# Performance work log

Hardware: AMD Instinct MI355X
Metric: run time of the kernel (lower is better)

## Reference

```python
import jax, jax.numpy as jnp
from jax import lax
import numpy as np

L = 2          # num_delimiter_layers
H = 8          # num q/kv heads
MIN_CL = 3
MAX_CL = 16

def rms_norm(x, w, eps=1e-6):
    return x * lax.rsqrt(jnp.mean(x * x, axis=-1, keepdims=True) + eps) * w

def rope(t):
    # t: [B, H, S, Dh], GPT-NeoX style half-split rotation, theta=10000
    Dh, S = t.shape[-1], t.shape[-2]
    half = Dh // 2
    inv = 1.0 / (10000.0 ** (jnp.arange(half, dtype=jnp.float32) / half))
    fr = jnp.arange(S, dtype=jnp.float32)[:, None] * inv  # [S, half]
    cos, sin = jnp.cos(fr), jnp.sin(fr)
    t1, t2 = t[..., :half], t[..., half:]
    return jnp.concatenate([t1 * cos - t2 * sin, t1 * sin + t2 * cos], axis=-1)

def chunk_ids_one(flags):
    # flags: [S] bool (probs > 0.5). Returns per-position chunk id and num chunks.
    S = flags.shape[0]
    # ends take value p+1 for flagged p; fallback to a single end at S-1 if none.
    has_end = jnp.zeros(S + 1, bool).at[1:].set(flags)
    fallback = jnp.zeros(S + 1, bool).at[S - 1].set(True)
    has_end = jnp.where(flags.any(), has_end, fallback)
    idx = jnp.where(has_end, jnp.arange(S + 1), S + 1)  # S+1 = sentinel > any cap
    nxt = lax.associative_scan(jnp.minimum, idx, reverse=True)  # nxt[e] = min end >= e
    def step(carry, t):
        cur_end, cid = carry
        def new(_):
            cap = jnp.minimum(t + MAX_CL, S)
            e = nxt[t + 1]                       # smallest end > t
            e = jnp.where(e <= cap, e, cap)
            e = jnp.where(e - t < MIN_CL, jnp.minimum(t + MIN_CL, S), e)
            return e, cid + 1
        new_end, new_cid = lax.cond(t == cur_end, new, lambda _: (cur_end, cid), None)
        return (new_end, new_cid), new_cid
    (_, last), ids = lax.scan(step, (jnp.int32(0), jnp.int32(-1)), jnp.arange(S, dtype=jnp.int32))
    return ids, last + 1

def _forward(x, ln1, Wq, Wk, Wv, Wo, ln2, W1, W2, head_w, head_b):
    B, S, D = x.shape
    Dh = D // H
    causal = jnp.tril(jnp.ones((S, S), bool))
    scale = 1.0 / np.sqrt(Dh)
    for l in range(L):
        h = rms_norm(x, ln1[l])
        def split_heads(t):
            return t.reshape(B, S, H, Dh).transpose(0, 2, 1, 3)
        q = rope(split_heads(h @ Wq[l]))
        k = rope(split_heads(h @ Wk[l]))
        v = split_heads(h @ Wv[l])
        scores = jnp.einsum('bhqd,bhkd->bhqk', q, k) * scale
        scores = jnp.where(causal, scores, jnp.finfo(scores.dtype).min)
        attn = jax.nn.softmax(scores, axis=-1)
        o = jnp.einsum('bhqk,bhkd->bhqd', attn, v)
        o = o.transpose(0, 2, 1, 3).reshape(B, S, D)
        x = x + o @ Wo[l]
        h = rms_norm(x, ln2[l])
        x = x + jax.nn.gelu(h @ W1[l], approximate=False) @ W2[l]
    logits = (x @ head_w).squeeze(-1) + head_b[0]
    probs = jax.nn.sigmoid(logits)
    chunk_len_loss = jnp.mean(jnp.sum(probs, axis=1))
    return x, probs, chunk_len_loss

def setup_inputs():
    key = jax.random.key(0)
    ks = jax.random.split(key, 10)
    B, S, D = 4, 2048, 512
    F = 4 * D
    sc = 0.02
    return {
        'x': jax.random.normal(ks[0], (B, S, D), jnp.float32),
        'x_ids': jax.random.randint(ks[1], (B, S), 0, 256),
        'ln1': jnp.ones((L, D), jnp.float32),
        'Wq': jax.random.normal(ks[2], (L, D, D), jnp.float32) * sc,
        'Wk': jax.random.normal(ks[3], (L, D, D), jnp.float32) * sc,
        'Wv': jax.random.normal(ks[4], (L, D, D), jnp.float32) * sc,
        'Wo': jax.random.normal(ks[5], (L, D, D), jnp.float32) * sc,
        'ln2': jnp.ones((L, D), jnp.float32),
        'W1': jax.random.normal(ks[6], (L, D, F), jnp.float32) * sc,
        'W2': jax.random.normal(ks[7], (L, F, D), jnp.float32) * sc,
        'head_w': jax.random.normal(ks[8], (D, 1), jnp.float32) * sc,
        'head_b': jnp.zeros((1,), jnp.float32),
    }

def reference(x, x_ids, ln1, Wq, Wk, Wv, Wo, ln2, W1, W2, head_w, head_b):
    B, S, D = x.shape
    x_t, probs, chunk_len_loss = _forward(x, ln1, Wq, Wk, Wv, Wo, ln2, W1, W2, head_w, head_b)
    flags = probs > 0.5
    ids, n_chunks = jax.vmap(chunk_ids_one)(flags)  # ids: [B,S] int32
    # chunks partition [0,S), so block-diagonal mask == chunk-id equality
    attention_masks = ids[:, :, None] == ids[:, None, :]
    # per-batch mean chunk length = S / num_chunks (lengths sum to S)
    avg_chunk_len = jnp.mean(jnp.float32(S) / n_chunks.astype(jnp.float32))
    return (x_t, x_ids, avg_chunk_len, attention_masks, chunk_len_loss)
```

## Files before the change

kernel.cpp:

```cpp
#include <hip/hip_runtime.h>
#include <math.h>

#define S_LEN 2048
#define DMODEL 512
#define NHEAD 8
#define DH 64
#define FDIM 2048

typedef unsigned short ushort_t;
typedef __attribute__((ext_vector_type(8))) short short8_t;
typedef __attribute__((ext_vector_type(4))) float float4_t;

#define MFMA16(a, b, c) __builtin_amdgcn_mfma_f32_16x16x32_bf16(a, b, c, 0, 0, 0)



__device__ __forceinline__ ushort_t f2bf(float x) {
    unsigned u = __float_as_uint(x);
    return (ushort_t)((u + 0x7fffu + ((u >> 16) & 1u)) >> 16);
}
__device__ __forceinline__ float bf2f(ushort_t h) {
    return __uint_as_float((unsigned)h << 16);
}
__device__ __forceinline__ float gelu_f(float x) {
    return 0.5f * x * (1.0f + erff(x * 0.70710678118654752440f));
}
__device__ __forceinline__ void gl_lds16(const void* g, void* l) {
    __builtin_amdgcn_global_load_lds(
        (const __attribute__((address_space(1))) void*)g,
        (__attribute__((address_space(3))) void*)l, 16, 0, 0);
}

__device__ __forceinline__ void stage_tile(const ushort_t* __restrict__ g, int rs,
                                           ushort_t* __restrict__ s, int w, int lane) {
    #pragma unroll
    for (int j = 0; j < 2; ++j) {
        const int c = (w * 2 + j) * 64 + lane;
        const int kk = c >> 8, row = (c >> 2) & 63, q = c & 3;
        const int qs = q ^ ((row >> 1) & 3);
        gl_lds16(g + (size_t)row * rs + kk * 32 + qs * 8, s + c * 8);
    }
}

__global__ void copy_init_k(const float* __restrict__ x, const int* __restrict__ x_ids,
                            float* __restrict__ out) {
    size_t i = (size_t)blockIdx.x * blockDim.x + threadIdx.x;
    float4* o4 = (float4*)out;
    o4[i] = ((const float4*)x)[i];
    if (i < 2048) {
        int4 id4 = ((const int4*)x_ids)[i];
        o4[1048576 + i] = make_float4((float)id4.x, (float)id4.y, (float)id4.z, (float)id4.w);
    }
    if (i == 0) { out[4202496] = 0.0f; out[20979713] = 0.0f; }
}

__global__ __launch_bounds__(256) void rope_tab_k(float2* __restrict__ tab) {
    const int i = blockIdx.x * 256 + threadIdx.x;
    const int s = i >> 5, f = i & 31;
    float inv = powf(10000.0f, -(float)f * (1.0f / 32.0f));
    float sn, cs;
    sincosf((float)s * inv, &sn, &cs);
    tab[i] = make_float2(cs, sn);
}

__global__ __launch_bounds__(256) void tsplit_all_k(const float* __restrict__ Wq,
                                                    const float* __restrict__ Wk,
                                                    const float* __restrict__ Wv,
                                                    const float* __restrict__ Wo,
                                                    const float* __restrict__ W1,
                                                    const float* __restrict__ W2,
                                                    ushort_t* __restrict__ wbuf) {
    __shared__ float T[32][33];
    const int bid = blockIdx.x;
    const int l = bid / 3072;
    const int r = bid % 3072;
    ushort_t* lb = wbuf + (size_t)l * 6291456;
    const float* W; ushort_t* Thi; ushort_t* Tlo; int K, N, ntn, rr;
    if (r < 768) {
        const int which = r >> 8; rr = r & 255;
        W = (which == 0 ? Wq : which == 1 ? Wk : Wv) + (size_t)l * 262144;
        Thi = lb + which * 262144; Tlo = lb + 786432 + which * 262144;
        K = 512; N = 512; ntn = 16;
    } else if (r < 1024) {
        rr = r - 768; W = Wo + (size_t)l * 262144;
        Thi = lb + 1572864; Tlo = lb + 1835008; K = 512; N = 512; ntn = 16;
    } else if (r < 2048) {
        rr = r - 1024; W = W1 + (size_t)l * 1048576;
        Thi = lb + 2097152; Tlo = lb + 3145728; K = 512; N = 2048; ntn = 64;
    } else {
        rr = r - 2048; W = W2 + (size_t)l * 1048576;
        Thi = lb + 4194304; Tlo = lb + 5242880; K = 2048; N = 512; ntn = 16;
    }
    const int n0 = (rr % ntn) * 32, k0 = (rr / ntn) * 32;
    const int tx = threadIdx.x & 31, ty = threadIdx.x >> 5;
    #pragma unroll
    for (int i = 0; i < 4; ++i)
        T[ty + 8 * i][tx] = W[(size_t)(k0 + ty + 8 * i) * N + n0 + tx];
    __syncthreads();
    #pragma unroll
    for (int i = 0; i < 4; ++i) {
        const int n = ty + 8 * i;
        float x = T[tx][n];
        ushort_t hi = f2bf(x);
        Thi[(size_t)(n0 + n) * K + k0 + tx] = hi;
        Tlo[(size_t)(n0 + n) * K + k0 + tx] = f2bf(x - bf2f(hi));
    }
}

__global__ __launch_bounds__(256) void rmsnorm_split_k(const float* __restrict__ x,
                                                       const float* __restrict__ w,
                                                       ushort_t* __restrict__ hhi,
                                                       ushort_t* __restrict__ hlo) {
    __shared__ float red[4];
    const int tid = threadIdx.x;
    const size_t row = blockIdx.x;
    const float* xr = x + row * DMODEL;
    float2 v = *(const float2*)(xr + tid * 2);
    float ss = v.x * v.x + v.y * v.y;
    #pragma unroll
    for (int off = 32; off; off >>= 1) ss += __shfl_down(ss, off);
    if ((tid & 63) == 0) red[tid >> 6] = ss;
    __syncthreads();
    float tot = red[0] + red[1] + red[2] + red[3];
    float rs = 1.0f / sqrtf(tot * (1.0f / 512.0f) + 1e-6f);
    float2 wv = *(const float2*)(w + tid * 2);
    float y0 = v.x * rs * wv.x, y1 = v.y * rs * wv.y;
    ushort_t h0 = f2bf(y0), h1 = f2bf(y1);
    ushort_t l0 = f2bf(y0 - bf2f(h0)), l1 = f2bf(y1 - bf2f(h1));
    *(unsigned*)(hhi + row * DMODEL + tid * 2) = ((unsigned)h1 << 16) | h0;
    *(unsigned*)(hlo + row * DMODEL + tid * 2) = ((unsigned)l1 << 16) | l0;
}

template<int EPI, int TN>
__global__ __launch_bounds__(256) void gemm_s(const ushort_t* __restrict__ Ahi,
                                              const ushort_t* __restrict__ Alo,
                                              const ushort_t* __restrict__ Bhi,
                                              const ushort_t* __restrict__ Blo,
                                              int K, int N,
                                              float* __restrict__ C,
                                              const float* __restrict__ Cin,
                                              ushort_t* __restrict__ Chi,
                                              ushort_t* __restrict__ Clo,
                                              ushort_t* __restrict__ oqh,
                                              ushort_t* __restrict__ oql,
                                              ushort_t* __restrict__ okh,
                                              ushort_t* __restrict__ okl,
                                              ushort_t* __restrict__ ovh,
                                              const float2* __restrict__ rtab) {
    constexpr int MT = (TN == 128) ? 4 : 2;
    __shared__ ushort_t sAhi[4096], sAlo[4096];
    __shared__ ushort_t sBhi[TN * 32], sBlo[TN * 32];
    const int tid = threadIdx.x;
    const int lane = tid & 63, w = tid >> 6;
    const int wm = (TN == 128) ? (w >> 1) : w;
    const int wn = (TN == 128) ? (w & 1) : 0;
    const int nbn = N / TN;
    const int id = blockIdx.x;
    const int jj = id >> 3;
    const int bm = (id & 7) * 8 + jj / nbn;
    const int bn = jj % nbn;
    const int sm = lane >> 2;
    const int sk = ((lane & 3) ^ ((sm >> 1) & 3)) * 8;
    const int fr = lane & 15;
    const int fq = lane >> 4;
    const int fko = (fq ^ ((fr >> 1) & 3)) * 8;

    float4_t acc[MT][4] = {};

    for (int kt = 0; kt < K; kt += 32) {
        #pragma unroll
        for (int j = 0; j < 2; ++j) {
            const int chunk = w * 2 + j;
            const int mr = chunk * 16 + sm;
            const size_t ga = (size_t)(bm * 128 + mr) * K + kt + sk;
            gl_lds16(Ahi + ga, &sAhi[chunk * 512]);
            gl_lds16(Alo + ga, &sAlo[chunk * 512]);
        }
        #pragma unroll
        for (int j = 0; j < TN / 64; ++j) {
            const int chunk = w * (TN / 64) + j;
            const int mr = chunk * 16 + sm;
            const size_t gb = (size_t)(bn * TN + mr) * K + kt + sk;
            gl_lds16(Bhi + gb, &sBhi[chunk * 512]);
            gl_lds16(Blo + gb, &sBlo[chunk * 512]);
        }
        __syncthreads();
        short8_t ah[MT], al[MT], bh[4], bl[4];
        #pragma unroll
        for (int t = 0; t < MT; ++t) {
            const int ao = (wm * (MT * 16) + t * 16 + fr) * 32 + fko;
            ah[t] = *(const short8_t*)&sAhi[ao];
            al[t] = *(const short8_t*)&sAlo[ao];
        }
        #pragma unroll
        for (int t = 0; t < 4; ++t) {
            const int bo = (wn * 64 + t * 16 + fr) * 32 + fko;
            bh[t] = *(const short8_t*)&sBhi[bo];
            bl[t] = *(const short8_t*)&sBlo[bo];
        }
        #pragma unroll
        for (int tm = 0; tm < MT; ++tm)
            #pragma unroll
            for (int tn = 0; tn < 4; ++tn) {
                acc[tm][tn] = MFMA16(ah[tm], bh[tn], acc[tm][tn]);
                acc[tm][tn] = MFMA16(al[tm], bh[tn], acc[tm][tn]);
                acc[tm][tn] = MFMA16(ah[tm], bl[tn], acc[tm][tn]);
            }
        __syncthreads();
    }

    if (EPI == 0) {
        const int cb = bn * 128 + wn * 64;
        const int mat = cb >> 9;
        const int hh = (cb >> 6) & 7;
        #pragma unroll
        for (int tm = 0; tm < MT; ++tm) {
            #pragma unroll
            for (int r = 0; r < 4; ++r) {
                const int mg = bm * 128 + wm * (MT * 16) + tm * 16 + fq * 4 + r;
                const int b = mg >> 11, s = mg & 2047;
                const int bhh = b * NHEAD + hh;
                if (mat < 2) {
                    ushort_t* dhi = (mat == 0) ? oqh : okh;
                    ushort_t* dlo = (mat == 0) ? oql : okl;
                    const size_t base = ((size_t)bhh * S_LEN + s) * DH;
                    #pragma unroll
                    for (int tn = 0; tn < 2; ++tn) {
                        const int d1 = tn * 16 + fr;
                        const float v1 = acc[tm][tn][r], v2 = acc[tm][tn + 2][r];
                        const float2 t = rtab[s * 32 + d1];
                        float r1 = v1 * t.x - v2 * t.y;
                        float r2 = v1 * t.y + v2 * t.x;
                        if (mat == 0) { r1 *= 0.125f; r2 *= 0.125f; }
                        ushort_t h1 = f2bf(r1), h2 = f2bf(r2);
                        dhi[base + d1]      = h1;
                        dlo[base + d1]      = f2bf(r1 - bf2f(h1));
                        dhi[base + d1 + 32] = h2;
                        dlo[base + d1 + 32] = f2bf(r2 - bf2f(h2));
                    }
                } else {
                    #pragma unroll
                    for (int tn = 0; tn < 4; ++tn) {
                        const int d = tn * 16 + fr;
                        const size_t off = ((size_t)bhh * DH + d) * S_LEN + s;
                        ovh[off] = f2bf(acc[tm][tn][r]);
                    }
                }
            }
        }
    } else {
        #pragma unroll
        for (int tm = 0; tm < MT; ++tm) {
            #pragma unroll
            for (int tn = 0; tn < 4; ++tn) {
                const int cb = bn * TN + wn * 64 + tn * 16;
                #pragma unroll
                for (int r = 0; r < 4; ++r) {
                    const int mg = bm * 128 + wm * (MT * 16) + tm * 16 + fq * 4 + r;
                    const float val = acc[tm][tn][r];
                    const size_t off = (size_t)mg * N + cb + fr;
                    if (EPI == 1) {
                        C[off] = Cin[off] + val;
                    } else {
                        const float g = gelu_f(val);
                        const ushort_t hi = f2bf(g);
                        Chi[off] = hi;
                        Clo[off] = f2bf(g - bf2f(hi));
                    }
                }
            }
        }
    }
}

__global__ __launch_bounds__(256) void attn_k(const ushort_t* __restrict__ qhi,
                                              const ushort_t* __restrict__ qlo,
                                              const ushort_t* __restrict__ khi,
                                              const ushort_t* __restrict__ klo,
                                              const ushort_t* __restrict__ vthi,
                                              ushort_t* __restrict__ Ohi,
                                              ushort_t* __restrict__ Olo) {
    __shared__ __align__(16) ushort_t sKh[4096], sKl[4096];
    __shared__ __align__(16) ushort_t sVh[4096], sPh[4096];
    const int tid = threadIdx.x, lane = tid & 63, w = tid >> 6;
    const int fr = lane & 15, fq = lane >> 4;
    const int fko = (fq ^ ((fr >> 1) & 3)) * 8;
    const int bidx = blockIdx.x;
    const int bh = bidx & 31;
    const int p = bidx >> 5;

    for (int half = 0; half < 2; ++half) {
        const int qt = half ? p : 31 - p;

        short8_t qfh[2], qfl[2];
        {
            const size_t base = ((size_t)bh * S_LEN + qt * 64 + w * 16 + fr) * DH + fq * 8;
            qfh[0] = *(const short8_t*)(qhi + base);
            qfh[1] = *(const short8_t*)(qhi + base + 32);
            qfl[0] = *(const short8_t*)(qlo + base);
            qfl[1] = *(const short8_t*)(qlo + base + 32);
        }

        float m_r[4], l_r[4];
        float4_t oacc[4] = {};
        #pragma unroll
        for (int r = 0; r < 4; ++r) { m_r[r] = -INFINITY; l_r[r] = 0.0f; }

        auto step = [&](const int kt, const bool diag) {
            __syncthreads();
            const size_t ko = ((size_t)bh * S_LEN + kt * 64) * DH;
            stage_tile(khi + ko, 64, sKh, w, lane);
            stage_tile(klo + ko, 64, sKl, w, lane);
            const size_t vo = (size_t)bh * DH * S_LEN + kt * 64;
            stage_tile(vthi + vo, S_LEN, sVh, w, lane);
            __syncthreads();

            float4_t sacc[4] = {};
            __builtin_amdgcn_s_setprio(1);
            #pragma unroll
            for (int kk = 0; kk < 2; ++kk) {
                #pragma unroll
                for (int n = 0; n < 4; ++n) {
                    const int bb = kk * 2048 + (n * 16 + fr) * 32 + fko;
                    short8_t kh2 = *(const short8_t*)&sKh[bb];
                    short8_t kl2 = *(const short8_t*)&sKl[bb];
                    sacc[n] = MFMA16(qfh[kk], kh2, sacc[n]);
                    sacc[n] = MFMA16(qfl[kk], kh2, sacc[n]);
                    sacc[n] = MFMA16(qfh[kk], kl2, sacc[n]);
                }
            }
            __builtin_amdgcn_s_setprio(0);

            #pragma unroll
            for (int r = 0; r < 4; ++r) {
                const int rowl = fq * 4 + r;
                const int qrow = w * 16 + rowl;
                const int psw = (qrow >> 1) & 3;
                float sv[4], mx = -INFINITY;
                #pragma unroll
                for (int n = 0; n < 4; ++n) {
                    sv[n] = sacc[n][r];
                    if (diag && (n * 16 + fr) > qrow) sv[n] = -1e30f;
                    mx = fmaxf(mx, sv[n]);
                }
                mx = fmaxf(mx, __shfl_xor(mx, 1));
                mx = fmaxf(mx, __shfl_xor(mx, 2));
                mx = fmaxf(mx, __shfl_xor(mx, 4));
                mx = fmaxf(mx, __shfl_xor(mx, 8));
                const float mn = fmaxf(m_r[r], mx);
                const float alp = __expf(m_r[r] - mn);
                m_r[r] = mn;
                float ls = 0.0f;
                #pragma unroll
                for (int n = 0; n < 4; ++n) {
                    const float pv = __expf(sv[n] - mn);
                    const int c0 = (n & 1) * 16 + fr;
                    const int idx = (n >> 1) * 2048 + qrow * 32 + ((c0 >> 3) ^ psw) * 8 + (c0 & 7);
                    sPh[idx] = f2bf(pv);
                    ls += pv;
                }
                ls += __shfl_xor(ls, 1);
                ls += __shfl_xor(ls, 2);
                ls += __shfl_xor(ls, 4);
                ls += __shfl_xor(ls, 8);
                l_r[r] = alp * l_r[r] + ls;
                #pragma unroll
                for (int n = 0; n < 4; ++n) oacc[n][r] *= alp;
            }

            __builtin_amdgcn_s_setprio(1);
            #pragma unroll
            for (int kkj = 0; kkj < 2; ++kkj) {
                short8_t ph = *(const short8_t*)&sPh[kkj * 2048 + (w * 16 + fr) * 32 + fko];
                #pragma unroll
                for (int n = 0; n < 4; ++n) {
                    short8_t vh = *(const short8_t*)&sVh[kkj * 2048 + (n * 16 + fr) * 32 + fko];
                    oacc[n] = MFMA16(ph, vh, oacc[n]);
                }
            }
            __builtin_amdgcn_s_setprio(0);
        };

        for (int kt = 0; kt < qt; ++kt) step(kt, false);
        step(qt, true);

        const int b = bh >> 3, hh = bh & 7;
        #pragma unroll
        for (int r = 0; r < 4; ++r) {
            const float inv_l = 1.0f / l_r[r];
            const int s = qt * 64 + w * 16 + fq * 4 + r;
            const size_t base = ((size_t)b * S_LEN + s) * DMODEL + hh * DH;
            #pragma unroll
            for (int n = 0; n < 4; ++n) {
                const float y = oacc[n][r] * inv_l;
                const ushort_t h = f2bf(y);
                Ohi[base + n * 16 + fr] = h;
                Olo[base + n * 16 + fr] = f2bf(y - bf2f(h));
            }
        }
    }
}

__global__ __launch_bounds__(256) void head_k(const float* __restrict__ x,
                                              const float* __restrict__ w,
                                              const float* __restrict__ b,
                                              float* __restrict__ probs) {
    const int tid = threadIdx.x;
    const int lane = tid & 63;
    const size_t row = (size_t)blockIdx.x * 4 + (tid >> 6);
    const float* xr = x + row * DMODEL;
    float acc = 0.0f;
    #pragma unroll
    for (int i = 0; i < 8; ++i) acc += xr[lane + i * 64] * w[lane + i * 64];
    #pragma unroll
    for (int off = 32; off; off >>= 1) acc += __shfl_down(acc, off);
    if (lane == 0)
        probs[row] = 1.0f / (1.0f + expf(-(acc + b[0])));
}

__global__ __launch_bounds__(256) void chunk_k(const float* __restrict__ probs,
                                               int* __restrict__ ids,
                                               float* __restrict__ avg_out,
                                               float* __restrict__ loss_out) {
    __shared__ ushort_t nxA[2052], nxB[2052];
    __shared__ ushort_t lift[10][2052];
    __shared__ float lred[4];
    __shared__ int anyf;
    const int b = blockIdx.x, tid = threadIdx.x;
    const float* pr = probs + (size_t)b * S_LEN;
    if (tid == 0) anyf = 0;
    __syncthreads();
    int loc = 0;
    float lsum = 0.0f;
    for (int t = tid; t < S_LEN; t += 256) {
        const float p = pr[t];
        loc |= (p > 0.5f) ? 1 : 0;
        lsum += p;
    }
    if (loc) atomicOr(&anyf, 1);
    #pragma unroll
    for (int off = 32; off; off >>= 1) lsum += __shfl_down(lsum, off);
    if ((tid & 63) == 0) lred[tid >> 6] = lsum;
    __syncthreads();
    if (tid == 0)
        atomicAdd(loss_out, (lred[0] + lred[1] + lred[2] + lred[3]) * 0.25f);
    const int any = anyf;
    for (int i = tid; i <= S_LEN; i += 256) {
        const bool he = any ? (i >= 1 && pr[i - 1] > 0.5f) : (i == S_LEN - 1);
        nxA[i] = he ? (ushort_t)i : (ushort_t)(S_LEN + 1);
    }
    __syncthreads();
    ushort_t* src = nxA;
    ushort_t* dst = nxB;
    for (int d = 1; d <= 2048; d <<= 1) {
        for (int i = tid; i <= S_LEN; i += 256) {
            ushort_t v = src[i];
            if (i + d <= S_LEN) { ushort_t u2 = src[i + d]; v = u2 < v ? u2 : v; }
            dst[i] = v;
        }
        __syncthreads();
        ushort_t* tmp = src; src = dst; dst = tmp;
    }
    for (int t = tid; t < S_LEN; t += 256) {
        int cap = t + 16; if (cap > S_LEN) cap = S_LEN;
        int e = src[t + 1];
        if (e > cap) e = cap;
        if (e - t < 3) { e = t + 3; if (e > S_LEN) e = S_LEN; }
        lift[0][t] = (ushort_t)e;
    }
    if (tid == 0) lift[0][S_LEN] = (ushort_t)S_LEN;
    __syncthreads();
    for (int j = 1; j < 10; ++j) {
        for (int t = tid; t <= S_LEN; t += 256)
            lift[j][t] = lift[j - 1][lift[j - 1][t]];
        __syncthreads();
    }
    for (int t = tid; t < S_LEN; t += 256) {
        int pos = 0, cid = 0;
        #pragma unroll
        for (int j = 9; j >= 0; --j) {
            const int p2 = lift[j][pos];
            if (p2 <= t) { pos = p2; cid += (1 << j); }
        }
        ids[(size_t)b * S_LEN + t] = cid;
        if (t == S_LEN - 1) atomicAdd(avg_out, 512.0f / (float)(cid + 1));
    }
}

__global__ __launch_bounds__(256) void masks_k(const int* __restrict__ ids,
                                               float* __restrict__ mask) {
    const int bq = blockIdx.x;
    const int b = bq >> 11;
    const int myid = ids[bq];
    const int* idr = ids + (size_t)b * S_LEN;
    float* mr = mask + (size_t)bq * S_LEN;
    for (int k = threadIdx.x; k < S_LEN; k += 256)
        mr[k] = (idr[k] == myid) ? 1.0f : 0.0f;
}

extern "C" void kernel_launch(void* const* d_in, const int* in_sizes, int n_in,
                              void* d_out, int out_size, void* d_ws, size_t ws_size,
                              hipStream_t stream) {
    (void)in_sizes; (void)n_in; (void)out_size; (void)ws_size;
    const float* x      = (const float*)d_in[0];
    const int*   x_ids  = (const int*)d_in[1];
    const float* ln1    = (const float*)d_in[2];
    const float* Wq     = (const float*)d_in[3];
    const float* Wk     = (const float*)d_in[4];
    const float* Wv     = (const float*)d_in[5];
    const float* Wo     = (const float*)d_in[6];
    const float* ln2    = (const float*)d_in[7];
    const float* W1     = (const float*)d_in[8];
    const float* W2     = (const float*)d_in[9];
    const float* head_w = (const float*)d_in[10];
    const float* head_b = (const float*)d_in[11];

    float* out = (float*)d_out;
    ushort_t* u = (ushort_t*)d_ws;
    ushort_t* qh   = u;
    ushort_t* ql   = u + 4194304;
    ushort_t* kh   = u + 8388608;
    ushort_t* kl   = u + 12582912;
    ushort_t* vth  = u + 16777216;
    ushort_t* ohi  = u + 25165824;
    ushort_t* olo  = u + 29360128;
    ushort_t* hhi  = u + 33554432;
    ushort_t* hlo  = u + 37748736;
    ushort_t* ffhi = u;
    ushort_t* fflo = u + 16777216;
    float*    probs = (float*)(u + 41943040);
    int*      ids   = (int*)(u + 41943040 + 16384);
    ushort_t* wbuf     = (ushort_t*)(out + 4202512);
    float2*   rope_tab = (float2*)(wbuf + 12582912);
    float* xbuf = out;

    copy_init_k<<<4096, 256, 0, stream>>>(x, x_ids, out);
    rope_tab_k<<<256, 256, 0, stream>>>(rope_tab);
    tsplit_all_k<<<6144, 256, 0, stream>>>(Wq, Wk, Wv, Wo, W1, W2, wbuf);

    for (int l = 0; l < 2; ++l) {
        ushort_t* lb = wbuf + (size_t)l * 6291456;
        ushort_t* qkvT_hi = lb;
        ushort_t* qkvT_lo = lb + 786432;
        ushort_t* woT_hi  = lb + 1572864;
        ushort_t* woT_lo  = lb + 1835008;
        ushort_t* w1T_hi  = lb + 2097152;
        ushort_t* w1T_lo  = lb + 3145728;
        ushort_t* w2T_hi  = lb + 4194304;
        ushort_t* w2T_lo  = lb + 5242880;

        rmsnorm_split_k<<<8192, 256, 0, stream>>>(xbuf, ln1 + l * DMODEL, hhi, hlo);
        gemm_s<0, 128><<<768, 256, 0, stream>>>(hhi, hlo, qkvT_hi, qkvT_lo, 512, 1536,
                                                nullptr, nullptr, nullptr, nullptr,
                                                qh, ql, kh, kl, vth, rope_tab);
        attn_k<<<512, 256, 0, stream>>>(qh, ql, kh, kl, vth, ohi, olo);
        gemm_s<1, 64><<<512, 256, 0, stream>>>(ohi, olo, woT_hi, woT_lo, 512, 512,
                                               xbuf, xbuf, nullptr, nullptr,
                                               nullptr, nullptr, nullptr, nullptr, nullptr, nullptr);
        rmsnorm_split_k<<<8192, 256, 0, stream>>>(xbuf, ln2 + l * DMODEL, hhi, hlo);
        gemm_s<2, 128><<<1024, 256, 0, stream>>>(hhi, hlo, w1T_hi, w1T_lo, 512, 2048,
                                                 nullptr, nullptr, ffhi, fflo,
                                                 nullptr, nullptr, nullptr, nullptr, nullptr, nullptr);
        gemm_s<1, 64><<<512, 256, 0, stream>>>(ffhi, fflo, w2T_hi, w2T_lo, 2048, 512,
                                               xbuf, xbuf, nullptr, nullptr,
                                               nullptr, nullptr, nullptr, nullptr, nullptr, nullptr);
    }

    head_k<<<2048, 256, 0, stream>>>(xbuf, head_w, head_b, probs);
    chunk_k<<<4, 256, 0, stream>>>(probs, ids, out + 4202496, out + 20979713);
    masks_k<<<8192, 256, 0, stream>>>(ids, out + 4202497);
}
```

Baseline: 815.1 us.

## Double-buffer LDS tiles in GEMM and attention kernels to overlap loads

Both the GEMM kernel and the attention kernel now keep two LDS buffers for their staged tiles. The next K-slice or K/V tile is issued into the alternate buffer while MFMAs run on the current one. This removes one barrier per iteration and hides global-to-LDS load latency behind compute. The cost is roughly double the LDS footprint, which may lower the number of resident blocks per CU.

```diff
diff --git a/kernel.cpp b/kernel.cpp
--- a/kernel.cpp
+++ b/kernel.cpp
@@ -148,8 +148,8 @@
                                               ushort_t* __restrict__ ovh,
                                               const float2* __restrict__ rtab) {
     constexpr int MT = (TN == 128) ? 4 : 2;
-    __shared__ ushort_t sAhi[4096], sAlo[4096];
-    __shared__ ushort_t sBhi[TN * 32], sBlo[TN * 32];
+    __shared__ __align__(16) ushort_t sAhi[2][4096], sAlo[2][4096];
+    __shared__ __align__(16) ushort_t sBhi[2][TN * 32], sBlo[2][TN * 32];
     const int tid = threadIdx.x;
     const int lane = tid & 63, w = tid >> 6;
     const int wm = (TN == 128) ? (w >> 1) : w;
@@ -165,38 +165,44 @@
     const int fq = lane >> 4;
     const int fko = (fq ^ ((fr >> 1) & 3)) * 8;
 
-    float4_t acc[MT][4] = {};
-
-    for (int kt = 0; kt < K; kt += 32) {
+    auto stage = [&](int buf, int kt) {
         #pragma unroll
         for (int j = 0; j < 2; ++j) {
             const int chunk = w * 2 + j;
             const int mr = chunk * 16 + sm;
             const size_t ga = (size_t)(bm * 128 + mr) * K + kt + sk;
-            gl_lds16(Ahi + ga, &sAhi[chunk * 512]);
-            gl_lds16(Alo + ga, &sAlo[chunk * 512]);
+            gl_lds16(Ahi + ga, &sAhi[buf][chunk * 512]);
+            gl_lds16(Alo + ga, &sAlo[buf][chunk * 512]);
         }
         #pragma unroll
         for (int j = 0; j < TN / 64; ++j) {
             const int chunk = w * (TN / 64) + j;
             const int mr = chunk * 16 + sm;
             const size_t gb = (size_t)(bn * TN + mr) * K + kt + sk;
-            gl_lds16(Bhi + gb, &sBhi[chunk * 512]);
-            gl_lds16(Blo + gb, &sBlo[chunk * 512]);
-        }
+            gl_lds16(Bhi + gb, &sBhi[buf][chunk * 512]);
+            gl_lds16(Blo + gb, &sBlo[buf][chunk * 512]);
+        }
+    };
+
+    float4_t acc[MT][4] = {};
+
+    stage(0, 0);
+    int cur = 0;
+    for (int kt = 0; kt < K; kt += 32) {
         __syncthreads();
+        if (kt + 32 < K) stage(cur ^ 1, kt + 32);
         short8_t ah[MT], al[MT], bh[4], bl[4];
         #pragma unroll
         for (int t = 0; t < MT; ++t) {
             const int ao = (wm * (MT * 16) + t * 16 + fr) * 32 + fko;
-            ah[t] = *(const short8_t*)&sAhi[ao];
-            al[t] = *(const short8_t*)&sAlo[ao];
+            ah[t] = *(const short8_t*)&sAhi[cur][ao];
+            al[t] = *(const short8_t*)&sAlo[cur][ao];
         }
         #pragma unroll
         for (int t = 0; t < 4; ++t) {
             const int bo = (wn * 64 + t * 16 + fr) * 32 + fko;
-            bh[t] = *(const short8_t*)&sBhi[bo];
-            bl[t] = *(const short8_t*)&sBlo[bo];
+            bh[t] = *(const short8_t*)&sBhi[cur][bo];
+            bl[t] = *(const short8_t*)&sBlo[cur][bo];
         }
         #pragma unroll
         for (int tm = 0; tm < MT; ++tm)
@@ -206,7 +212,7 @@
                 acc[tm][tn] = MFMA16(al[tm], bh[tn], acc[tm][tn]);
                 acc[tm][tn] = MFMA16(ah[tm], bl[tn], acc[tm][tn]);
             }
-        __syncthreads();
+        cur ^= 1;
     }
 
     if (EPI == 0) {
@@ -280,14 +286,22 @@
                                               const ushort_t* __restrict__ vthi,
                                               ushort_t* __restrict__ Ohi,
                                               ushort_t* __restrict__ Olo) {
-    __shared__ __align__(16) ushort_t sKh[4096], sKl[4096];
-    __shared__ __align__(16) ushort_t sVh[4096], sPh[4096];
+    __shared__ __align__(16) ushort_t sKh[2][4096], sKl[2][4096];
+    __shared__ __align__(16) ushort_t sVh[2][4096], sPh[4096];
     const int tid = threadIdx.x, lane = tid & 63, w = tid >> 6;
     const int fr = lane & 15, fq = lane >> 4;
     const int fko = (fq ^ ((fr >> 1) & 3)) * 8;
     const int bidx = blockIdx.x;
     const int bh = bidx & 31;
     const int p = bidx >> 5;
+
+    auto stage3 = [&](int buf, int kt) {
+        const size_t ko = ((size_t)bh * S_LEN + kt * 64) * DH;
+        stage_tile(khi + ko, 64, sKh[buf], w, lane);
+        stage_tile(klo + ko, 64, sKl[buf], w, lane);
+        const size_t vo = (size_t)bh * DH * S_LEN + kt * 64;
+        stage_tile(vthi + vo, S_LEN, sVh[buf], w, lane);
+    };
 
     for (int half = 0; half < 2; ++half) {
         const int qt = half ? p : 31 - p;
@@ -306,14 +320,14 @@
         #pragma unroll
         for (int r = 0; r < 4; ++r) { m_r[r] = -INFINITY; l_r[r] = 0.0f; }
 
-        auto step = [&](const int kt, const bool diag) {
+        __syncthreads();
+        stage3(0, 0);
+        int cur = 0;
+
+        for (int kt = 0; kt <= qt; ++kt) {
+            const bool diag = (kt == qt);
             __syncthreads();
-            const size_t ko = ((size_t)bh * S_LEN + kt * 64) * DH;
-            stage_tile(khi + ko, 64, sKh, w, lane);
-            stage_tile(klo + ko, 64, sKl, w, lane);
-            const size_t vo = (size_t)bh * DH * S_LEN + kt * 64;
-            stage_tile(vthi + vo, S_LEN, sVh, w, lane);
-            __syncthreads();
+            if (kt < qt) stage3(cur ^ 1, kt + 1);
 
             float4_t sacc[4] = {};
             __builtin_amdgcn_s_setprio(1);
@@ -322,8 +336,8 @@
                 #pragma unroll
                 for (int n = 0; n < 4; ++n) {
                     const int bb = kk * 2048 + (n * 16 + fr) * 32 + fko;
-                    short8_t kh2 = *(const short8_t*)&sKh[bb];
-                    short8_t kl2 = *(const short8_t*)&sKl[bb];
+                    short8_t kh2 = *(const short8_t*)&sKh[cur][bb];
+                    short8_t kl2 = *(const short8_t*)&sKl[cur][bb];
                     sacc[n] = MFMA16(qfh[kk], kh2, sacc[n]);
                     sacc[n] = MFMA16(qfl[kk], kh2, sacc[n]);
                     sacc[n] = MFMA16(qfh[kk], kl2, sacc[n]);
@@ -374,15 +388,13 @@
                 short8_t ph = *(const short8_t*)&sPh[kkj * 2048 + (w * 16 + fr) * 32 + fko];
                 #pragma unroll
                 for (int n = 0; n < 4; ++n) {
-                    short8_t vh = *(const short8_t*)&sVh[kkj * 2048 + (n * 16 + fr) * 32 + fko];
+                    short8_t vh = *(const short8_t*)&sVh[cur][kkj * 2048 + (n * 16 + fr) * 32 + fko];
                     oacc[n] = MFMA16(ph, vh, oacc[n]);
                 }
             }
             __builtin_amdgcn_s_setprio(0);
-        };
-
-        for (int kt = 0; kt < qt; ++kt) step(kt, false);
-        step(qt, true);
+            cur ^= 1;
+        }
 
         const int b = bh >> 3, hh = bh & 7;
         #pragma unroll
```

Measured after the change: 783.4 us. -3.9%, faster.
